# Kernel optimization log

Hardware: AMD Instinct MI355X
Metric: run time of the kernel (lower is better)

## Reference

```python
import jax, jax.numpy as jnp
import numpy as np

N, D, C = 131072, 64, 256  # points, latent dim, SOM cells
EPS = 1e-08
TEMP_LO = 0.001


def _cdist(a, b):
    # Euclidean pairwise distance, matching torch.cdist (p=2).
    d2 = (jnp.sum(a * a, axis=1)[:, None]
          + jnp.sum(b * b, axis=1)[None, :]
          - 2.0 * (a @ b.T))
    return jnp.sqrt(jnp.maximum(d2, 0.0))


def setup_inputs() -> dict:
    key = jax.random.key(0)
    kx, kp, kg = jax.random.split(key, 3)
    x = jax.random.normal(kx, (N, D), dtype=jnp.float32)
    prototypes = jax.random.normal(kp, (C, D), dtype=jnp.float32)
    grid_pos = jax.random.normal(kg, (C, D), dtype=jnp.float32)
    gate_logits = jnp.zeros((C,), dtype=jnp.float32)
    # temp_raw = logit(init_temperature) with init_temperature = 0.95
    temp_raw = jnp.array([np.log(0.95 / 0.05)], dtype=jnp.float32)
    return {"x": x, "prototypes": prototypes, "grid_pos": grid_pos,
            "gate_logits": gate_logits, "temp_raw": temp_raw}


def reference(x, prototypes, grid_pos, gate_logits, temp_raw):
    # temperature = sigmoid(temp_raw) * (1 - 0.001) + 0.001, a scalar
    temp = jax.nn.sigmoid(temp_raw[0]) * (1.0 - TEMP_LO) + TEMP_LO
    gate = jax.nn.sigmoid(gate_logits)[None, :]            # [1, C]
    d_total = _cdist(x, prototypes) + _cdist(x, grid_pos)  # [N, C]
    w = jnp.exp(-d_total / temp)
    w = w / (jnp.sum(w, axis=-1, keepdims=True) + EPS)
    w = w * gate
    w = w / (jnp.sum(w, axis=-1, keepdims=True) + EPS)
    blended = w @ prototypes                               # [N, D]
    return blended, w
```

## Files before the change

kernel.cpp:

```cpp
#include <hip/hip_runtime.h>

#define N_PTS 131072
#define DIM   64
#define CELLS 256
#define EPSF  1e-8f
#define WS_ALPHA 1024

__global__ void prep_kernel(const float* __restrict__ prototypes,
                            const float* __restrict__ grid_pos,
                            const float* __restrict__ gate_logits,
                            const float* __restrict__ temp_raw,
                            float* __restrict__ ws) {
    const int c = threadIdx.x;
    const float* p = prototypes + c * DIM;
    const float* g = grid_pos   + c * DIM;
    float pn = 0.f, gn = 0.f;
#pragma unroll
    for (int k = 0; k < DIM; ++k) {
        pn = fmaf(p[k], p[k], pn);
        gn = fmaf(g[k], g[k], gn);
    }
    ws[c]             = pn;
    ws[CELLS + c]     = gn;
    ws[2 * CELLS + c] = 1.f / (1.f + expf(-gate_logits[c]));
    if (c == 0) {
        float sg   = 1.f / (1.f + expf(-temp_raw[0]));
        float temp = sg * (1.f - 0.001f) + 0.001f;
        ws[3 * CELLS] = -1.4426950408889634f / temp;
    }
}

__global__ __launch_bounds__(256, 2)
void dist_kernel(const float* __restrict__ x,
                 const float* __restrict__ P,
                 const float* __restrict__ G,
                 const float* __restrict__ ws,
                 float* __restrict__ w_out,
                 float* __restrict__ alpha_out) {
    extern __shared__ float lds[];
    float* xT = lds;
    float* PT = lds + 8192;
    float* GT = lds + 12288;

    const int t  = threadIdx.x;
    const int pr = t >> 4;
    const int cr = t & 15;
    const int pbase = blockIdx.x * 128;

    {
        const int pt = t & 127;
        const int qh = t >> 7;
        const float4* xp = reinterpret_cast<const float4*>(
            x + (size_t)(pbase + pt) * DIM);
        float xpart = 0.f;
#pragma unroll
        for (int j = 0; j < 8; ++j) {
            const int q = qh * 8 + j;
            float4 v = xp[q];
            xpart += v.x*v.x + v.y*v.y + v.z*v.z + v.w*v.w;
#pragma unroll
            for (int jj = 0; jj < 4; ++jj) {
                const int k = 4 * q + jj;
                xT[k * 128 + 4 * ((pt >> 2) ^ (k >> 1)) + (pt & 3)] = (&v.x)[jj];
            }
        }
        PT[qh * 128 + pt] = xpart;
    }
    __syncthreads();
    float xn[8];
#pragma unroll
    for (int i = 0; i < 8; ++i) {
        const int p = ((i < 4) ? 0 : 64) + 4 * pr + (i & 3);
        xn[i] = PT[p] + PT[128 + p];
    }
    __syncthreads();

    const float cscale = ws[3 * CELLS];
    float s1r[8], sgr[8];
#pragma unroll
    for (int i = 0; i < 8; ++i) { s1r[i] = 0.f; sgr[i] = 0.f; }

#pragma unroll 1
    for (int cc = 0; cc < 4; ++cc) {
        const int cc0 = cc * 64;
        {
            const int cl = t & 63;
            const int qb = t >> 6;
            const float4* P4 = reinterpret_cast<const float4*>(
                P + (size_t)(cc0 + cl) * DIM);
            const float4* G4 = reinterpret_cast<const float4*>(
                G + (size_t)(cc0 + cl) * DIM);
#pragma unroll
            for (int j = 0; j < 4; ++j) {
                const int q = 4 * qb + j;
                float4 v = P4[q];
                float4 u = G4[q];
#pragma unroll
                for (int jj = 0; jj < 4; ++jj) {
                    const int k   = 4 * q + jj;
                    const int off = k * 64 + 4 * ((cl >> 2) ^ (k & 15)) + (cl & 3);
                    PT[off] = (&v.x)[jj];
                    GT[off] = (&u.x)[jj];
                }
            }
        }
        __syncthreads();

        float accP[8][4], accG[8][4];
#pragma unroll
        for (int i = 0; i < 8; ++i)
#pragma unroll
            for (int j = 0; j < 4; ++j) { accP[i][j] = 0.f; accG[i][j] = 0.f; }

#pragma unroll 8
        for (int k = 0; k < 64; ++k) {
            const float4 xf0 = *reinterpret_cast<const float4*>(
                &xT[k * 128 + 4 * (pr ^ (k >> 1))]);
            const float4 xf1 = *reinterpret_cast<const float4*>(
                &xT[k * 128 + 4 * ((pr + 16) ^ (k >> 1))]);
            const float4 pf = *reinterpret_cast<const float4*>(
                &PT[k * 64 + 4 * (cr ^ (k & 15))]);
            const float4 gf = *reinterpret_cast<const float4*>(
                &GT[k * 64 + 4 * (cr ^ (k & 15))]);
#pragma unroll
            for (int i = 0; i < 4; ++i) {
                const float a = (&xf0.x)[i];
                const float b = (&xf1.x)[i];
#pragma unroll
                for (int j = 0; j < 4; ++j) {
                    const float pv = (&pf.x)[j];
                    const float gv = (&gf.x)[j];
                    accP[i][j]     = fmaf(a, pv, accP[i][j]);
                    accG[i][j]     = fmaf(a, gv, accG[i][j]);
                    accP[4 + i][j] = fmaf(b, pv, accP[4 + i][j]);
                    accG[4 + i][j] = fmaf(b, gv, accG[4 + i][j]);
                }
            }
        }
        __syncthreads();

        const float4 pnv = *reinterpret_cast<const float4*>(ws + cc0 + 4 * cr);
        const float4 gnv = *reinterpret_cast<const float4*>(ws + CELLS + cc0 + 4 * cr);
        const float4 gav = *reinterpret_cast<const float4*>(ws + 2 * CELLS + cc0 + 4 * cr);
        float* ttile = PT;
#pragma unroll
        for (int i = 0; i < 8; ++i) {
            const int p = ((i < 4) ? 0 : 64) + 4 * pr + (i & 3);
            float s1p = 0.f, sgp = 0.f;
            float tt[4];
#pragma unroll
            for (int j = 0; j < 4; ++j) {
                float dp2 = fmaf(-2.f, accP[i][j], xn[i] + (&pnv.x)[j]);
                float dg2 = fmaf(-2.f, accG[i][j], xn[i] + (&gnv.x)[j]);
                float d   = sqrtf(fmaxf(dp2, 0.f)) + sqrtf(fmaxf(dg2, 0.f));
                float e   = exp2f(d * cscale);
                s1p += e;
                float tv = e * (&gav.x)[j];
                sgp += tv;
                tt[j] = tv;
            }
            *reinterpret_cast<float4*>(&ttile[p * 64 + 4 * (cr ^ (p & 15))]) =
                make_float4(tt[0], tt[1], tt[2], tt[3]);
            s1p += __shfl_xor(s1p, 1);  sgp += __shfl_xor(sgp, 1);
            s1p += __shfl_xor(s1p, 2);  sgp += __shfl_xor(sgp, 2);
            s1p += __shfl_xor(s1p, 4);  sgp += __shfl_xor(sgp, 4);
            s1p += __shfl_xor(s1p, 8);  sgp += __shfl_xor(sgp, 8);
            s1r[i] += s1p;
            sgr[i] += sgp;
        }
        __syncthreads();

#pragma unroll
        for (int j = 0; j < 8; ++j) {
            const int f   = j * 256 + t;
            const int row = f >> 4;
            const int q2  = f & 15;
            float4 v = *reinterpret_cast<const float4*>(
                &ttile[row * 64 + 4 * (q2 ^ (row & 15))]);
            *reinterpret_cast<float4*>(
                w_out + (size_t)(pbase + row) * CELLS + cc0 + 4 * q2) = v;
        }
        __syncthreads();
    }

    if (cr == 0) {
#pragma unroll
        for (int i = 0; i < 8; ++i) {
            const int p = ((i < 4) ? 0 : 64) + 4 * pr + (i & 3);
            const float A  = s1r[i] + EPSF;
            const float s2 = sgr[i] / A;
            alpha_out[pbase + p] = 1.f / (A * (s2 + EPSF));
        }
    }
}

__global__ __launch_bounds__(256, 2)
void blend_kernel(float* __restrict__ w,
                  const float* __restrict__ P,
                  const float* __restrict__ alpha_in,
                  float* __restrict__ bl) {
    extern __shared__ float lds2[];
    float* wT = lds2;
    float* Pt = lds2 + 8192;

    const int t  = threadIdx.x;
    const int pr = t & 31;
    const int dr = t >> 5;
    const size_t pbase = (size_t)blockIdx.x * 256;

    const float al = alpha_in[pbase + t];

    float acc[8][8];
#pragma unroll
    for (int i = 0; i < 8; ++i)
#pragma unroll
        for (int j = 0; j < 8; ++j) acc[i][j] = 0.f;

#pragma unroll 1
    for (int cc = 0; cc < 8; ++cc) {
        const int cc0 = cc * 32;
        {
            float* wrow = w + (pbase + t) * CELLS + cc0;
#pragma unroll
            for (int j = 0; j < 8; ++j) {
                float4 v = *reinterpret_cast<const float4*>(wrow + 4 * j);
                v.x *= al; v.y *= al; v.z *= al; v.w *= al;
                *reinterpret_cast<float4*>(wrow + 4 * j) = v;
#pragma unroll
                for (int jj = 0; jj < 4; ++jj) {
                    const int r = 4 * j + jj;
                    wT[r * 256 + 4 * ((t >> 2) ^ r) + (t & 3)] = (&v.x)[jj];
                }
            }
        }
#pragma unroll
        for (int j = 0; j < 2; ++j) {
            const int f  = j * 256 + t;
            const int cl = f & 31;
            const int q  = (f >> 5) & 15;
            float4 v = *reinterpret_cast<const float4*>(
                P + (size_t)(cc0 + cl) * DIM + 4 * q);
            *reinterpret_cast<float4*>(&Pt[cl * 64 + 4 * (q ^ (cl & 15))]) = v;
        }
        __syncthreads();

#pragma unroll 4
        for (int k = 0; k < 32; ++k) {
            const float4 wf0 = *reinterpret_cast<const float4*>(
                &wT[k * 256 + 4 * (pr ^ k)]);
            const float4 wf1 = *reinterpret_cast<const float4*>(
                &wT[k * 256 + 4 * ((32 + pr) ^ k)]);
            const float4 pf0 = *reinterpret_cast<const float4*>(
                &Pt[k * 64 + 4 * ((2 * dr) ^ (k & 15))]);
            const float4 pf1 = *reinterpret_cast<const float4*>(
                &Pt[k * 64 + 4 * ((2 * dr + 1) ^ (k & 15))]);
#pragma unroll
            for (int i = 0; i < 4; ++i) {
                const float a = (&wf0.x)[i];
                const float b = (&wf1.x)[i];
#pragma unroll
                for (int j = 0; j < 4; ++j) {
                    const float p0 = (&pf0.x)[j];
                    const float p1 = (&pf1.x)[j];
                    acc[i][j]         = fmaf(a, p0, acc[i][j]);
                    acc[i][4 + j]     = fmaf(a, p1, acc[i][4 + j]);
                    acc[4 + i][j]     = fmaf(b, p0, acc[4 + i][j]);
                    acc[4 + i][4 + j] = fmaf(b, p1, acc[4 + i][4 + j]);
                }
            }
        }
        __syncthreads();
    }

#pragma unroll
    for (int i = 0; i < 8; ++i) {
        const int p = ((i < 4) ? 0 : 128) + 4 * pr + (i & 3);
        float* orow = bl + (pbase + p) * DIM + 8 * dr;
        *reinterpret_cast<float4*>(orow) =
            make_float4(acc[i][0], acc[i][1], acc[i][2], acc[i][3]);
        *reinterpret_cast<float4*>(orow + 4) =
            make_float4(acc[i][4], acc[i][5], acc[i][6], acc[i][7]);
    }
}

extern "C" void kernel_launch(void* const* d_in, const int* in_sizes, int n_in,
                              void* d_out, int out_size, void* d_ws, size_t ws_size,
                              hipStream_t stream) {
    const float* x           = (const float*)d_in[0];
    const float* prototypes  = (const float*)d_in[1];
    const float* grid_pos    = (const float*)d_in[2];
    const float* gate_logits = (const float*)d_in[3];
    const float* temp_raw    = (const float*)d_in[4];
    float*       out         = (float*)d_out;
    float*       blended     = out;
    float*       w           = out + (size_t)N_PTS * DIM;
    float*       ws          = (float*)d_ws;
    float*       alpha       = ws + WS_ALPHA;

    (void)hipFuncSetAttribute((const void*)dist_kernel,
                              hipFuncAttributeMaxDynamicSharedMemorySize, 65536);

    prep_kernel<<<1, CELLS, 0, stream>>>(prototypes, grid_pos, gate_logits,
                                         temp_raw, ws);
    dist_kernel<<<N_PTS / 128, 256, 65536, stream>>>(x, prototypes, grid_pos,
                                                     ws, w, alpha);
    blend_kernel<<<N_PTS / 256, 256, 40960, stream>>>(w, prototypes, alpha,
                                                      blended);
}
```

Baseline: 413.1 us.

## Enlarge dist register tile to 8x8 and software-pipeline blend kernel loads

The distance kernel now processes 128 cells per pass with an 8x8 per-thread accumulator tile, splitting K into two 32-wide panels. This raises FMA-to-LDS-load ratio and halves the number of cell chunks. Row sums go through LDS instead of registers. The blend kernel prefetches the next w/P chunk into registers while computing the current one and raises launch bounds to 3 blocks per CU. The costs are much higher register pressure in dist (128 accumulators plus a 64-entry tt array) that may cause spills, and extra LDS.

```diff
diff --git a/kernel.cpp b/kernel.cpp
--- a/kernel.cpp
+++ b/kernel.cpp
@@ -38,163 +38,198 @@
                  float* __restrict__ w_out,
                  float* __restrict__ alpha_out) {
     extern __shared__ float lds[];
-    float* xT = lds;
-    float* PT = lds + 8192;
-    float* GT = lds + 12288;
+    float* xT  = lds;
+    float* PT  = lds + 8192;
+    float* GT  = lds + 12288;
+    float* xnL = lds + 16384;
+    float* s1L = lds + 16512;
+    float* sgL = lds + 16768;
+    float* ttile = PT;
 
     const int t  = threadIdx.x;
     const int pr = t >> 4;
     const int cr = t & 15;
     const int pbase = blockIdx.x * 128;
 
+#define PTS(i) ((i) < 4 ? 4 * pr + (i) : 64 + 4 * pr + ((i) - 4))
+
     {
-        const int pt = t & 127;
-        const int qh = t >> 7;
+        const int pt   = t & 127;
+        const int half = t >> 7;
         const float4* xp = reinterpret_cast<const float4*>(
-            x + (size_t)(pbase + pt) * DIM);
+            x + (size_t)(pbase + pt) * DIM) + half * 8;
         float xpart = 0.f;
 #pragma unroll
         for (int j = 0; j < 8; ++j) {
-            const int q = qh * 8 + j;
-            float4 v = xp[q];
-            xpart += v.x*v.x + v.y*v.y + v.z*v.z + v.w*v.w;
+            float4 v = xp[j];
+            xpart += v.x * v.x + v.y * v.y + v.z * v.z + v.w * v.w;
 #pragma unroll
             for (int jj = 0; jj < 4; ++jj) {
-                const int k = 4 * q + jj;
-                xT[k * 128 + 4 * ((pt >> 2) ^ (k >> 1)) + (pt & 3)] = (&v.x)[jj];
-            }
-        }
-        PT[qh * 128 + pt] = xpart;
+                const int k = 32 * half + 4 * j + jj;
+                xT[k * 128 + 4 * ((pt >> 2) ^ (k & 31)) + (pt & 3)] = (&v.x)[jj];
+            }
+        }
+        PT[half * 128 + pt] = xpart;
     }
     __syncthreads();
-    float xn[8];
-#pragma unroll
-    for (int i = 0; i < 8; ++i) {
-        const int p = ((i < 4) ? 0 : 64) + 4 * pr + (i & 3);
-        xn[i] = PT[p] + PT[128 + p];
-    }
+    if (t < 128) xnL[t] = PT[t] + PT[128 + t];
     __syncthreads();
 
     const float cscale = ws[3 * CELLS];
-    float s1r[8], sgr[8];
-#pragma unroll
-    for (int i = 0; i < 8; ++i) { s1r[i] = 0.f; sgr[i] = 0.f; }
 
 #pragma unroll 1
-    for (int cc = 0; cc < 4; ++cc) {
-        const int cc0 = cc * 64;
-        {
-            const int cl = t & 63;
-            const int qb = t >> 6;
-            const float4* P4 = reinterpret_cast<const float4*>(
-                P + (size_t)(cc0 + cl) * DIM);
-            const float4* G4 = reinterpret_cast<const float4*>(
-                G + (size_t)(cc0 + cl) * DIM);
-#pragma unroll
-            for (int j = 0; j < 4; ++j) {
-                const int q = 4 * qb + j;
-                float4 v = P4[q];
-                float4 u = G4[q];
-#pragma unroll
-                for (int jj = 0; jj < 4; ++jj) {
-                    const int k   = 4 * q + jj;
-                    const int off = k * 64 + 4 * ((cl >> 2) ^ (k & 15)) + (cl & 3);
-                    PT[off] = (&v.x)[jj];
-                    GT[off] = (&u.x)[jj];
+    for (int ch = 0; ch < 2; ++ch) {
+        const int cc0 = ch * 128;
+        float aP[8][8], aG[8][8];
+#pragma unroll
+        for (int i = 0; i < 8; ++i)
+#pragma unroll
+            for (int j = 0; j < 8; ++j) { aP[i][j] = 0.f; aG[i][j] = 0.f; }
+
+#pragma unroll 1
+        for (int pan = 0; pan < 2; ++pan) {
+            const int k0 = pan * 32;
+            {
+                const int cl = t & 127;
+                const int kh = t >> 7;
+                const float4* Pp = reinterpret_cast<const float4*>(
+                    P + (size_t)(cc0 + cl) * DIM + k0 + 16 * kh);
+                const float4* Gp = reinterpret_cast<const float4*>(
+                    G + (size_t)(cc0 + cl) * DIM + k0 + 16 * kh);
+#pragma unroll
+                for (int j = 0; j < 4; ++j) {
+                    float4 v = Pp[j];
+                    float4 u = Gp[j];
+#pragma unroll
+                    for (int jj = 0; jj < 4; ++jj) {
+                        const int kk  = 16 * kh + 4 * j + jj;
+                        const int off = kk * 128 + 4 * ((cl >> 2) ^ kk) + (cl & 3);
+                        PT[off] = (&v.x)[jj];
+                        GT[off] = (&u.x)[jj];
+                    }
                 }
             }
-        }
-        __syncthreads();
-
-        float accP[8][4], accG[8][4];
-#pragma unroll
-        for (int i = 0; i < 8; ++i)
-#pragma unroll
-            for (int j = 0; j < 4; ++j) { accP[i][j] = 0.f; accG[i][j] = 0.f; }
-
-#pragma unroll 8
-        for (int k = 0; k < 64; ++k) {
-            const float4 xf0 = *reinterpret_cast<const float4*>(
-                &xT[k * 128 + 4 * (pr ^ (k >> 1))]);
-            const float4 xf1 = *reinterpret_cast<const float4*>(
-                &xT[k * 128 + 4 * ((pr + 16) ^ (k >> 1))]);
-            const float4 pf = *reinterpret_cast<const float4*>(
-                &PT[k * 64 + 4 * (cr ^ (k & 15))]);
-            const float4 gf = *reinterpret_cast<const float4*>(
-                &GT[k * 64 + 4 * (cr ^ (k & 15))]);
-#pragma unroll
-            for (int i = 0; i < 4; ++i) {
-                const float a = (&xf0.x)[i];
-                const float b = (&xf1.x)[i];
-#pragma unroll
-                for (int j = 0; j < 4; ++j) {
-                    const float pv = (&pf.x)[j];
-                    const float gv = (&gf.x)[j];
-                    accP[i][j]     = fmaf(a, pv, accP[i][j]);
-                    accG[i][j]     = fmaf(a, gv, accG[i][j]);
-                    accP[4 + i][j] = fmaf(b, pv, accP[4 + i][j]);
-                    accG[4 + i][j] = fmaf(b, gv, accG[4 + i][j]);
+            __syncthreads();
+
+#pragma unroll 4
+            for (int kk = 0; kk < 32; ++kk) {
+                const int k = k0 + kk;
+                const float4 xf0 = *reinterpret_cast<const float4*>(
+                    &xT[k * 128 + 4 * (pr ^ (k & 31))]);
+                const float4 xf1 = *reinterpret_cast<const float4*>(
+                    &xT[k * 128 + 4 * ((16 + pr) ^ (k & 31))]);
+                const float4 pf0 = *reinterpret_cast<const float4*>(
+                    &PT[kk * 128 + 4 * (cr ^ kk)]);
+                const float4 pf1 = *reinterpret_cast<const float4*>(
+                    &PT[kk * 128 + 4 * ((16 + cr) ^ kk)]);
+                const float4 gf0 = *reinterpret_cast<const float4*>(
+                    &GT[kk * 128 + 4 * (cr ^ kk)]);
+                const float4 gf1 = *reinterpret_cast<const float4*>(
+                    &GT[kk * 128 + 4 * ((16 + cr) ^ kk)]);
+#pragma unroll
+                for (int i = 0; i < 4; ++i) {
+                    const float a = (&xf0.x)[i];
+                    const float b = (&xf1.x)[i];
+#pragma unroll
+                    for (int j = 0; j < 4; ++j) {
+                        const float p0 = (&pf0.x)[j];
+                        const float p1 = (&pf1.x)[j];
+                        const float g0 = (&gf0.x)[j];
+                        const float g1 = (&gf1.x)[j];
+                        aP[i][j]         = fmaf(a, p0, aP[i][j]);
+                        aP[i][4 + j]     = fmaf(a, p1, aP[i][4 + j]);
+                        aP[4 + i][j]     = fmaf(b, p0, aP[4 + i][j]);
+                        aP[4 + i][4 + j] = fmaf(b, p1, aP[4 + i][4 + j]);
+                        aG[i][j]         = fmaf(a, g0, aG[i][j]);
+                        aG[i][4 + j]     = fmaf(a, g1, aG[i][4 + j]);
+                        aG[4 + i][j]     = fmaf(b, g0, aG[4 + i][j]);
+                        aG[4 + i][4 + j] = fmaf(b, g1, aG[4 + i][4 + j]);
+                    }
                 }
             }
-        }
-        __syncthreads();
-
-        const float4 pnv = *reinterpret_cast<const float4*>(ws + cc0 + 4 * cr);
-        const float4 gnv = *reinterpret_cast<const float4*>(ws + CELLS + cc0 + 4 * cr);
-        const float4 gav = *reinterpret_cast<const float4*>(ws + 2 * CELLS + cc0 + 4 * cr);
-        float* ttile = PT;
+            __syncthreads();
+        }
+
+        const float4 pn0 = *reinterpret_cast<const float4*>(ws + cc0 + 4 * cr);
+        const float4 pn1 = *reinterpret_cast<const float4*>(ws + cc0 + 64 + 4 * cr);
+        const float4 gn0 = *reinterpret_cast<const float4*>(ws + CELLS + cc0 + 4 * cr);
+        const float4 gn1 = *reinterpret_cast<const float4*>(ws + CELLS + cc0 + 64 + 4 * cr);
+        const float4 ga0 = *reinterpret_cast<const float4*>(ws + 2 * CELLS + cc0 + 4 * cr);
+        const float4 ga1 = *reinterpret_cast<const float4*>(ws + 2 * CELLS + cc0 + 64 + 4 * cr);
+        float tt[8][8];
 #pragma unroll
         for (int i = 0; i < 8; ++i) {
-            const int p = ((i < 4) ? 0 : 64) + 4 * pr + (i & 3);
-            float s1p = 0.f, sgp = 0.f;
-            float tt[4];
-#pragma unroll
-            for (int j = 0; j < 4; ++j) {
-                float dp2 = fmaf(-2.f, accP[i][j], xn[i] + (&pnv.x)[j]);
-                float dg2 = fmaf(-2.f, accG[i][j], xn[i] + (&gnv.x)[j]);
+            const float xnv = xnL[PTS(i)];
+            float s1 = 0.f, sg = 0.f;
+#pragma unroll
+            for (int j = 0; j < 8; ++j) {
+                const float pnj = (j < 4) ? (&pn0.x)[j] : (&pn1.x)[j - 4];
+                const float gnj = (j < 4) ? (&gn0.x)[j] : (&gn1.x)[j - 4];
+                const float gaj = (j < 4) ? (&ga0.x)[j] : (&ga1.x)[j - 4];
+                float dp2 = fmaf(-2.f, aP[i][j], xnv + pnj);
+                float dg2 = fmaf(-2.f, aG[i][j], xnv + gnj);
                 float d   = sqrtf(fmaxf(dp2, 0.f)) + sqrtf(fmaxf(dg2, 0.f));
                 float e   = exp2f(d * cscale);
-                s1p += e;
-                float tv = e * (&gav.x)[j];
-                sgp += tv;
-                tt[j] = tv;
-            }
+                s1 += e;
+                float tv = e * gaj;
+                sg += tv;
+                tt[i][j] = tv;
+            }
+            s1 += __shfl_xor(s1, 1);  sg += __shfl_xor(sg, 1);
+            s1 += __shfl_xor(s1, 2);  sg += __shfl_xor(sg, 2);
+            s1 += __shfl_xor(s1, 4);  sg += __shfl_xor(sg, 4);
+            s1 += __shfl_xor(s1, 8);  sg += __shfl_xor(sg, 8);
+            if (cr == 0) { s1L[ch * 128 + PTS(i)] = s1; sgL[ch * 128 + PTS(i)] = sg; }
+        }
+
+#pragma unroll
+        for (int i = 0; i < 8; ++i) {
+            const int p = PTS(i);
             *reinterpret_cast<float4*>(&ttile[p * 64 + 4 * (cr ^ (p & 15))]) =
-                make_float4(tt[0], tt[1], tt[2], tt[3]);
-            s1p += __shfl_xor(s1p, 1);  sgp += __shfl_xor(sgp, 1);
-            s1p += __shfl_xor(s1p, 2);  sgp += __shfl_xor(sgp, 2);
-            s1p += __shfl_xor(s1p, 4);  sgp += __shfl_xor(sgp, 4);
-            s1p += __shfl_xor(s1p, 8);  sgp += __shfl_xor(sgp, 8);
-            s1r[i] += s1p;
-            sgr[i] += sgp;
-        }
-        __syncthreads();
-
+                make_float4(tt[i][0], tt[i][1], tt[i][2], tt[i][3]);
+        }
+        __syncthreads();
 #pragma unroll
         for (int j = 0; j < 8; ++j) {
-            const int f   = j * 256 + t;
+            const int f = j * 256 + t;
             const int row = f >> 4;
-            const int q2  = f & 15;
+            const int q   = f & 15;
             float4 v = *reinterpret_cast<const float4*>(
-                &ttile[row * 64 + 4 * (q2 ^ (row & 15))]);
+                &ttile[row * 64 + 4 * (q ^ (row & 15))]);
             *reinterpret_cast<float4*>(
-                w_out + (size_t)(pbase + row) * CELLS + cc0 + 4 * q2) = v;
-        }
-        __syncthreads();
-    }
-
-    if (cr == 0) {
+                w_out + (size_t)(pbase + row) * CELLS + cc0 + 4 * q) = v;
+        }
+        __syncthreads();
 #pragma unroll
         for (int i = 0; i < 8; ++i) {
-            const int p = ((i < 4) ? 0 : 64) + 4 * pr + (i & 3);
-            const float A  = s1r[i] + EPSF;
-            const float s2 = sgr[i] / A;
-            alpha_out[pbase + p] = 1.f / (A * (s2 + EPSF));
-        }
-    }
+            const int p = PTS(i);
+            *reinterpret_cast<float4*>(&ttile[p * 64 + 4 * (cr ^ (p & 15))]) =
+                make_float4(tt[i][4], tt[i][5], tt[i][6], tt[i][7]);
+        }
+        __syncthreads();
+#pragma unroll
+        for (int j = 0; j < 8; ++j) {
+            const int f = j * 256 + t;
+            const int row = f >> 4;
+            const int q   = f & 15;
+            float4 v = *reinterpret_cast<const float4*>(
+                &ttile[row * 64 + 4 * (q ^ (row & 15))]);
+            *reinterpret_cast<float4*>(
+                w_out + (size_t)(pbase + row) * CELLS + cc0 + 64 + 4 * q) = v;
+        }
+        __syncthreads();
+    }
+
+    if (t < 128) {
+        const float A  = s1L[t] + s1L[128 + t] + EPSF;
+        const float sg = sgL[t] + sgL[128 + t];
+        const float s2 = sg / A;
+        alpha_out[pbase + t] = 1.f / (A * (s2 + EPSF));
+    }
+#undef PTS
 }
 
-__global__ __launch_bounds__(256, 2)
+__global__ __launch_bounds__(256, 3)
 void blend_kernel(float* __restrict__ w,
                   const float* __restrict__ P,
                   const float* __restrict__ alpha_in,
@@ -216,34 +251,42 @@
 #pragma unroll
         for (int j = 0; j < 8; ++j) acc[i][j] = 0.f;
 
-#pragma unroll 1
-    for (int cc = 0; cc < 8; ++cc) {
-        const int cc0 = cc * 32;
-        {
-            float* wrow = w + (pbase + t) * CELLS + cc0;
-#pragma unroll
-            for (int j = 0; j < 8; ++j) {
-                float4 v = *reinterpret_cast<const float4*>(wrow + 4 * j);
-                v.x *= al; v.y *= al; v.z *= al; v.w *= al;
-                *reinterpret_cast<float4*>(wrow + 4 * j) = v;
-#pragma unroll
-                for (int jj = 0; jj < 4; ++jj) {
-                    const int r = 4 * j + jj;
-                    wT[r * 256 + 4 * ((t >> 2) ^ r) + (t & 3)] = (&v.x)[jj];
-                }
-            }
-        }
+    auto LOADW = [&](float4* wr, float4* pp, int cc0) {
+        const float* wrow = w + (pbase + t) * CELLS + cc0;
+#pragma unroll
+        for (int j = 0; j < 8; ++j)
+            wr[j] = *reinterpret_cast<const float4*>(wrow + 4 * j);
 #pragma unroll
         for (int j = 0; j < 2; ++j) {
             const int f  = j * 256 + t;
             const int cl = f & 31;
             const int q  = (f >> 5) & 15;
-            float4 v = *reinterpret_cast<const float4*>(
+            pp[j] = *reinterpret_cast<const float4*>(
                 P + (size_t)(cc0 + cl) * DIM + 4 * q);
-            *reinterpret_cast<float4*>(&Pt[cl * 64 + 4 * (q ^ (cl & 15))]) = v;
-        }
-        __syncthreads();
-
+        }
+    };
+    auto STAGE = [&](float4* wr, float4* pp, int cc0) {
+        float* wrow = w + (pbase + t) * CELLS + cc0;
+#pragma unroll
+        for (int j = 0; j < 8; ++j) {
+            float4 v = wr[j];
+            v.x *= al; v.y *= al; v.z *= al; v.w *= al;
+            *reinterpret_cast<float4*>(wrow + 4 * j) = v;
+#pragma unroll
+            for (int jj = 0; jj < 4; ++jj) {
+                const int r = 4 * j + jj;
+                wT[r * 256 + 4 * ((t >> 2) ^ r) + (t & 3)] = (&v.x)[jj];
+            }
+        }
+#pragma unroll
+        for (int j = 0; j < 2; ++j) {
+            const int f  = j * 256 + t;
+            const int cl = f & 31;
+            const int q  = (f >> 5) & 15;
+            *reinterpret_cast<float4*>(&Pt[cl * 64 + 4 * (q ^ (cl & 15))]) = pp[j];
+        }
+    };
+    auto KLOOP = [&]() {
 #pragma unroll 4
         for (int k = 0; k < 32; ++k) {
             const float4 wf0 = *reinterpret_cast<const float4*>(
@@ -269,6 +312,22 @@
                 }
             }
         }
+    };
+
+    float4 wA[8], pA[2], wB[8], pB[2];
+    LOADW(wA, pA, 0);
+
+#pragma unroll 1
+    for (int cp = 0; cp < 4; ++cp) {
+        STAGE(wA, pA, (2 * cp) * 32);
+        __syncthreads();
+        LOADW(wB, pB, (2 * cp + 1) * 32);
+        KLOOP();
+        __syncthreads();
+        STAGE(wB, pB, (2 * cp + 1) * 32);
+        __syncthreads();
+        if (cp < 3) LOADW(wA, pA, (2 * cp + 2) * 32);
+        KLOOP();
         __syncthreads();
     }
 
@@ -298,11 +357,11 @@
     float*       alpha       = ws + WS_ALPHA;
 
     (void)hipFuncSetAttribute((const void*)dist_kernel,
-                              hipFuncAttributeMaxDynamicSharedMemorySize, 65536);
+                              hipFuncAttributeMaxDynamicSharedMemorySize, 69632);
 
     prep_kernel<<<1, CELLS, 0, stream>>>(prototypes, grid_pos, gate_logits,
                                          temp_raw, ws);
-    dist_kernel<<<N_PTS / 128, 256, 65536, stream>>>(x, prototypes, grid_pos,
+    dist_kernel<<<N_PTS / 128, 256, 68096, stream>>>(x, prototypes, grid_pos,
                                                      ws, w, alpha);
     blend_kernel<<<N_PTS / 256, 256, 40960, stream>>>(w, prototypes, alpha,
                                                       blended);
```

Result: slower. 480.3 us (+16.3%).
